# Kernel optimization log

Measured on AMD Instinct MI355X. Metric: run time of the kernel, lower is better.

The kernel has to match this reference:

```python
import jax, jax.numpy as jnp
import numpy as np


def setup_inputs() -> dict:
    key = jax.random.key(0)
    kq, kk, kv = jax.random.split(key, 3)
    B, L, S, H, E, D = 2, 2048, 2048, 16, 64, 64
    return {
        "queries": jax.random.normal(kq, (B, L, H, E), dtype=jnp.float32),
        "keys": jax.random.normal(kk, (B, S, H, E), dtype=jnp.float32),
        "values": jax.random.normal(kv, (B, S, H, D), dtype=jnp.float32),
    }


def reference(queries, keys, values):
    # FullAttention forward (mask_flag=False, dropout=0.0 -> identity)
    E = queries.shape[-1]
    scale = 1.0 / jnp.sqrt(jnp.asarray(E, dtype=queries.dtype))
    # scores: [B, H, L, S]
    scores = jnp.einsum('blhe,bshe->bhls', queries, keys)
    A = jax.nn.softmax(scale * scores, axis=-1)
    # output: [B, L, H, D]
    V = jnp.einsum('bhls,bshd->blhd', A, values)
    return V
```

## Files before the change

### kernel.cpp

```cpp
#include <hip/hip_runtime.h>
#include <hip/hip_bf16.h>
#include <string.h>


#define NB 2
#define LL 2048
#define SS 2048
#define HH 16
#define EE 64
#define DD 64
#define KVB 64
#define NT (SS / KVB)
#define NWG2 (NB * HH * (LL / 64))

typedef _Float16 f16x8 __attribute__((ext_vector_type(8)));
typedef float f32x4 __attribute__((ext_vector_type(4)));
typedef float f32x16 __attribute__((ext_vector_type(16)));
typedef unsigned uint2v __attribute__((ext_vector_type(2)));
typedef unsigned uint4v __attribute__((ext_vector_type(4)));
typedef const __attribute__((address_space(1))) void* gas_p;
typedef __attribute__((address_space(3))) void* las_p;

__device__ __forceinline__ unsigned pk2h(float a, float b) {
    auto h = __builtin_amdgcn_cvt_pkrtz(a, b);
    unsigned u;
    __builtin_memcpy(&u, &h, 4);
    return u;
}

__device__ __forceinline__ float fexp2(float x) {
#if defined(__has_builtin) && __has_builtin(__builtin_amdgcn_exp2f)
    return __builtin_amdgcn_exp2f(x);
#else
    return exp2f(x);
#endif
}

__device__ __forceinline__ void gll16(const void* g, void* l) {
    __builtin_amdgcn_global_load_lds((gas_p)g, (las_p)l, 16, 0, 0);
}

__device__ __forceinline__ uint2v plswap(unsigned a, unsigned b) {
#if defined(__has_builtin) && __has_builtin(__builtin_amdgcn_permlane32_swap)
    return __builtin_amdgcn_permlane32_swap(a, b, false, false);
#else
    unsigned ax = (unsigned)__shfl_xor((int)a, 32);
    unsigned bx = (unsigned)__shfl_xor((int)b, 32);
    int l32 = (int)(threadIdx.x & 32);
    uint2v r;
    r[0] = l32 ? bx : a;
    r[1] = l32 ? b : ax;
    return r;
#endif
}

__device__ __forceinline__ float fbits(unsigned u) {
    float f; __builtin_memcpy(&f, &u, 4); return f;
}
__device__ __forceinline__ unsigned ubits(float f) {
    unsigned u; __builtin_memcpy(&u, &f, 4); return u;
}
__device__ __forceinline__ float xsum32(float x) {
    uint2v r = plswap(ubits(x), ubits(x));
    return fbits(r[0]) + fbits(r[1]);
}

__global__ __launch_bounds__(256) void prepKV(const float* __restrict__ K,
                                              const float* __restrict__ V,
                                              unsigned short* __restrict__ Kh,
                                              unsigned short* __restrict__ Vth) {
    const int NTILE = NB * HH * NT;
    const bool isV = blockIdx.x >= NTILE;
    const int tile = blockIdx.x & (NTILE - 1);
    const int it = tile & (NT - 1);
    const int bh = tile >> 5;
    const int b = bh >> 4, h = bh & 15;
    const int t = threadIdx.x;

    if (!isV) {
        const int s = t >> 2, ec = t & 3;
        const float* src = K + (((size_t)b * SS + it * KVB + s) * HH + h) * EE + ec * 16;
        f32x4 x0 = ((const f32x4*)src)[0];
        f32x4 x1 = ((const f32x4*)src)[1];
        f32x4 x2 = ((const f32x4*)src)[2];
        f32x4 x3 = ((const f32x4*)src)[3];
        uint4v c0, c1;
        c0.x = pk2h(x0[0], x0[1]); c0.y = pk2h(x0[2], x0[3]);
        c0.z = pk2h(x1[0], x1[1]); c0.w = pk2h(x1[2], x1[3]);
        c1.x = pk2h(x2[0], x2[1]); c1.y = pk2h(x2[2], x2[3]);
        c1.z = pk2h(x3[0], x3[1]); c1.w = pk2h(x3[2], x3[3]);
        char* dst = (char*)Kh + (size_t)tile * 8192;
        const int sw = (s & 7) << 4;
        *(uint4v*)(dst + ((s * 128 + ec * 32) ^ sw)) = c0;
        *(uint4v*)(dst + ((s * 128 + ec * 32 + 16) ^ sw)) = c1;
    } else {
        __shared__ float Vt[64 * 68];
        {
            const int s = t >> 2, dc = t & 3;
            const float* src = V + (((size_t)b * SS + it * KVB + s) * HH + h) * DD + dc * 16;
            f32x4 x0 = ((const f32x4*)src)[0];
            f32x4 x1 = ((const f32x4*)src)[1];
            f32x4 x2 = ((const f32x4*)src)[2];
            f32x4 x3 = ((const f32x4*)src)[3];
            float* row = Vt + s * 68 + dc * 16;
            ((f32x4*)row)[0] = x0; ((f32x4*)row)[1] = x1;
            ((f32x4*)row)[2] = x2; ((f32x4*)row)[3] = x3;
        }
        __syncthreads();
        {
            const int d = t >> 2, sc = t & 3;
            float w[16];
#pragma unroll
            for (int j = 0; j < 16; ++j) w[j] = Vt[(sc * 16 + j) * 68 + d];
            uint4v c0, c1;
            c0.x = pk2h(w[0], w[1]); c0.y = pk2h(w[2], w[3]);
            c0.z = pk2h(w[4], w[5]); c0.w = pk2h(w[6], w[7]);
            c1.x = pk2h(w[8], w[9]); c1.y = pk2h(w[10], w[11]);
            c1.z = pk2h(w[12], w[13]); c1.w = pk2h(w[14], w[15]);
            char* dst = (char*)Vth + (size_t)tile * 8192;
            const int sw = (d & 7) << 4;
            *(uint4v*)(dst + ((d * 128 + sc * 32) ^ sw)) = c0;
            *(uint4v*)(dst + ((d * 128 + sc * 32 + 16) ^ sw)) = c1;
        }
    }
}

__global__ __launch_bounds__(256, 4) void fattn9(const unsigned short* __restrict__ Kh,
                                                 const unsigned short* __restrict__ Vth,
                                                 const float* __restrict__ Q,
                                                 float* __restrict__ O) {
    __shared__ __align__(16) char LB[32768];
    __shared__ float lsh[4][32];
    char* K0s = LB;
    char* K1s = LB + 8192;
    char* V0s = LB + 16384;
    char* V1s = LB + 24576;

    const int tid = threadIdx.x;
    const int lane = tid & 63;
    const int wid = tid >> 6;
    const int ln = lane & 31;
    const int hi = lane >> 5;
    const int qg = wid >> 1;
    const int sh = wid & 1;

    const int bid0 = blockIdx.x;
    const int bid = (bid0 & 7) * (NWG2 >> 3) + (bid0 >> 3);
    const int bh = bid >> 5;
    const int qt = bid & 31;
    const int b = bh >> 4, h = bh & 15;
    const int qrow = qt * 64 + qg * 32 + ln;

    const float qs = 0.125f * 1.44269504088896340736f;
    const float* qptr = Q + (((size_t)b * LL + qrow) * HH + h) * EE + hi * 8;
    f16x8 qf[4];
#pragma unroll
    for (int ks = 0; ks < 4; ++ks) {
        f32x4 a0 = *(const f32x4*)(qptr + ks * 16);
        f32x4 a1 = *(const f32x4*)(qptr + ks * 16 + 4);
        union { f16x8 v; unsigned u[4]; } cv;
        cv.u[0] = pk2h(a0[0] * qs, a0[1] * qs);
        cv.u[1] = pk2h(a0[2] * qs, a0[3] * qs);
        cv.u[2] = pk2h(a1[0] * qs, a1[1] * qs);
        cv.u[3] = pk2h(a1[2] * qs, a1[3] * qs);
        qf[ks] = cv.v;
    }

    f32x16 o0, o1;
#pragma unroll
    for (int i = 0; i < 16; ++i) { o0[i] = 0.f; o1[i] = 0.f; }
    float l = 0.f;

    const char* Kg = (const char*)Kh + (size_t)bh * (NT * 8192);
    const char* Vg = (const char*)Vth + (size_t)bh * (NT * 8192);

    auto STAGE = [&](int it, char* Ks, char* Vs) {
        const size_t off = (size_t)it * 8192 + wid * 2048 + lane * 16;
        gll16(Kg + off, Ks + wid * 2048);
        gll16(Kg + off + 1024, Ks + wid * 2048 + 1024);
        gll16(Vg + off, Vs + wid * 2048);
        gll16(Vg + off + 1024, Vs + wid * 2048 + 1024);
    };

    const int swz = (ln & 7) << 4;
    const int srow = sh * 32 + ln;
    const int vcol = sh * 64;

    auto COMPUTE = [&](const char* Ks, const char* Vs) {
        f32x16 st;
#pragma unroll
        for (int i = 0; i < 16; ++i) st[i] = 0.f;
        __builtin_amdgcn_s_setprio(1);
#pragma unroll
        for (int ks = 0; ks < 4; ++ks) {
            f16x8 kf = *(const f16x8*)(Ks + ((srow * 128 + ks * 32 + hi * 16) ^ swz));
            st = __builtin_amdgcn_mfma_f32_32x32x16_f16(kf, qf[ks], st, 0, 0, 0);
        }
        __builtin_amdgcn_s_setprio(0);

        float t0 = 0.f, t1 = 0.f, t2 = 0.f, t3 = 0.f;
#pragma unroll
        for (int r = 0; r < 16; r += 4) {
            st[r] = fexp2(st[r]);
            st[r + 1] = fexp2(st[r + 1]);
            st[r + 2] = fexp2(st[r + 2]);
            st[r + 3] = fexp2(st[r + 3]);
            t0 += st[r]; t1 += st[r + 1]; t2 += st[r + 2]; t3 += st[r + 3];
        }
        l += (t0 + t1) + (t2 + t3);

        {
            uint2v r0 = plswap(pk2h(st[0], st[1]), pk2h(st[4], st[5]));
            uint2v r1 = plswap(pk2h(st[2], st[3]), pk2h(st[6], st[7]));
            union { f16x8 v; unsigned u[4]; } w;
            w.u[0] = r0[0]; w.u[1] = r1[0]; w.u[2] = r0[1]; w.u[3] = r1[1];
            f16x8 v0 = *(const f16x8*)(Vs + ((ln * 128 + vcol + hi * 16) ^ swz));
            f16x8 v1 = *(const f16x8*)(Vs + (((32 + ln) * 128 + vcol + hi * 16) ^ swz));
            __builtin_amdgcn_s_setprio(1);
            o0 = __builtin_amdgcn_mfma_f32_32x32x16_f16(v0, w.v, o0, 0, 0, 0);
            o1 = __builtin_amdgcn_mfma_f32_32x32x16_f16(v1, w.v, o1, 0, 0, 0);
            __builtin_amdgcn_s_setprio(0);
        }
        {
            uint2v r2 = plswap(pk2h(st[8], st[9]), pk2h(st[12], st[13]));
            uint2v r3 = plswap(pk2h(st[10], st[11]), pk2h(st[14], st[15]));
            union { f16x8 v; unsigned u[4]; } w;
            w.u[0] = r2[0]; w.u[1] = r3[0]; w.u[2] = r2[1]; w.u[3] = r3[1];
            f16x8 v0 = *(const f16x8*)(Vs + ((ln * 128 + vcol + 32 + hi * 16) ^ swz));
            f16x8 v1 = *(const f16x8*)(Vs + (((32 + ln) * 128 + vcol + 32 + hi * 16) ^ swz));
            __builtin_amdgcn_s_setprio(1);
            o0 = __builtin_amdgcn_mfma_f32_32x32x16_f16(v0, w.v, o0, 0, 0, 0);
            o1 = __builtin_amdgcn_mfma_f32_32x32x16_f16(v1, w.v, o1, 0, 0, 0);
            __builtin_amdgcn_s_setprio(0);
        }
    };

    STAGE(0, K0s, V0s);
    __syncthreads();
    for (int it = 0; it < NT; it += 2) {
        if (it + 1 < NT) STAGE(it + 1, K1s, V1s);
        COMPUTE(K0s, V0s);
        __syncthreads();
        if (it + 2 < NT) STAGE(it + 2, K0s, V0s);
        COMPUTE(K1s, V1s);
        __syncthreads();
    }

    l = xsum32(l);
    if (hi == 0) lsh[wid][ln] = l;
    __syncthreads();
    const float lo = lsh[wid ^ 1][ln];
    const float lstar = l + lo;

    float* pbuf = (float*)LB + qg * (32 * 65);
    if (sh == 1) {
#pragma unroll
        for (int r = 0; r < 16; ++r) {
            const int d = (r & 3) + 8 * (r >> 2) + 4 * hi;
            pbuf[ln * 65 + d] = o0[r];
            pbuf[ln * 65 + 32 + d] = o1[r];
        }
    }
    __syncthreads();
    if (sh == 0) {
        const float invl = 1.f / lstar;
        float* optr = O + (((size_t)b * LL + qrow) * HH + h) * DD;
#pragma unroll
        for (int t = 0; t < 4; ++t) {
            f32x4 w0, w1;
#pragma unroll
            for (int i = 0; i < 4; ++i) {
                const int d = t * 8 + hi * 4 + i;
                w0[i] = (o0[4 * t + i] + pbuf[ln * 65 + d]) * invl;
                w1[i] = (o1[4 * t + i] + pbuf[ln * 65 + 32 + d]) * invl;
            }
            *(f32x4*)(optr + t * 8 + hi * 4) = w0;
            *(f32x4*)(optr + 32 + t * 8 + hi * 4) = w1;
        }
    }
}

typedef unsigned u2f __attribute__((ext_vector_type(2)));
__global__ __launch_bounds__(256) void fattn1(const float* __restrict__ Q,
                                              const float* __restrict__ K,
                                              const float* __restrict__ V,
                                              float* __restrict__ O) {
    __shared__ __align__(16) short Klds[KVB * 64];
    __shared__ __align__(16) short Vtlds[64 * KVB];
    __shared__ __align__(16) short Plds[4][16 * 64];

    const int tid = threadIdx.x;
    const int lane = tid & 63;
    const int wid = tid >> 6;
    const int g = (lane >> 4) & 3;
    const int c = lane & 15;

    const int bid = blockIdx.x;
    const int bh = bid >> 5;
    const int qt = bid & 31;
    const int b = bh >> 4;
    const int h = bh & 15;
    const int q0 = qt * 64;

    const int qrow = q0 + wid * 16 + c;
    const float* qptr = Q + (((size_t)b * LL + qrow) * HH + h) * EE;
    const float qs = 0.125f * 1.44269504088896340736f;
    f16x8 qf[2];
#pragma unroll
    for (int kk = 0; kk < 2; ++kk) {
        f32x4 a0 = *(const f32x4*)(qptr + kk * 32 + g * 8);
        f32x4 a1 = *(const f32x4*)(qptr + kk * 32 + g * 8 + 4);
        union { f16x8 v; unsigned u[4]; } cv;
        cv.u[0] = pk2h(a0[0] * qs, a0[1] * qs);
        cv.u[1] = pk2h(a0[2] * qs, a0[3] * qs);
        cv.u[2] = pk2h(a1[0] * qs, a1[1] * qs);
        cv.u[3] = pk2h(a1[2] * qs, a1[3] * qs);
        qf[kk] = cv.v;
    }

    f32x4 osacc[4];
    const f32x4 fzero = {0.f, 0.f, 0.f, 0.f};
#pragma unroll
    for (int i = 0; i < 4; ++i) osacc[i] = fzero;
    float m_run = -1e30f;
    float l_run = 0.f;

    const int km = tid & 15;
    const int kr = tid >> 4;

    for (int it = 0; it < NT; ++it) {
        const int s_glob = it * KVB;
        f32x4 kreg[4];
#pragma unroll
        for (int p = 0; p < 4; ++p) {
            int s = kr + p * 16;
            kreg[p] = *(const f32x4*)(K + (((size_t)b * SS + s_glob + s) * HH + h) * EE + km * 4);
        }
        f32x4 vreg[4];
#pragma unroll
        for (int p = 0; p < 4; ++p) {
            int s = kr * 4 + p;
            vreg[p] = *(const f32x4*)(V + (((size_t)b * SS + s_glob + s) * HH + h) * DD + km * 4);
        }
        __syncthreads();
#pragma unroll
        for (int p = 0; p < 4; ++p) {
            int s = kr + p * 16;
            u2f w;
            w.x = pk2h(kreg[p][0], kreg[p][1]);
            w.y = pk2h(kreg[p][2], kreg[p][3]);
            int byte = (s * 128 + km * 8) ^ ((s & 7) << 4);
            *(u2f*)((char*)Klds + byte) = w;
        }
#pragma unroll
        for (int i = 0; i < 4; ++i) {
            int d = km * 4 + i;
            u2f w;
            w.x = pk2h(vreg[0][i], vreg[1][i]);
            w.y = pk2h(vreg[2][i], vreg[3][i]);
            int byte = (d * 128 + kr * 8) ^ ((d & 7) << 4);
            *(u2f*)((char*)Vtlds + byte) = w;
        }
        __syncthreads();

        f32x4 stv[4];
#pragma unroll
        for (int fr = 0; fr < 4; ++fr) stv[fr] = fzero;
#pragma unroll
        for (int fr = 0; fr < 4; ++fr) {
            int s = fr * 16 + c;
            f16x8 kf0 = *(const f16x8*)((const char*)Klds + ((s * 128 + 16 * g) ^ ((s & 7) << 4)));
            stv[fr] = __builtin_amdgcn_mfma_f32_16x16x32_f16(kf0, qf[0], stv[fr], 0, 0, 0);
            f16x8 kf1 = *(const f16x8*)((const char*)Klds + ((s * 128 + 64 + 16 * g) ^ ((s & 7) << 4)));
            stv[fr] = __builtin_amdgcn_mfma_f32_16x16x32_f16(kf1, qf[1], stv[fr], 0, 0, 0);
        }

        float pmax = stv[0][0];
#pragma unroll
        for (int fr = 0; fr < 4; ++fr)
#pragma unroll
            for (int r = 0; r < 4; ++r) pmax = fmaxf(pmax, stv[fr][r]);
        pmax = fmaxf(pmax, __shfl_xor(pmax, 16));
        pmax = fmaxf(pmax, __shfl_xor(pmax, 32));
        float mnew = fmaxf(m_run, pmax);
        float alpha = fexp2(m_run - mnew);
        float tsum = 0.f;
#pragma unroll
        for (int fr = 0; fr < 4; ++fr)
#pragma unroll
            for (int r = 0; r < 4; ++r) {
                float e = fexp2(stv[fr][r] - mnew);
                stv[fr][r] = e;
                tsum += e;
            }
        tsum += __shfl_xor(tsum, 16);
        tsum += __shfl_xor(tsum, 32);
        l_run = l_run * alpha + tsum;
        m_run = mnew;
#pragma unroll
        for (int fr = 0; fr < 4; ++fr)
#pragma unroll
            for (int r = 0; r < 4; ++r) osacc[fr][r] *= alpha;

        short* plb = &Plds[wid][0];
#pragma unroll
        for (int fr = 0; fr < 4; ++fr) {
            u2f w;
            w.x = pk2h(stv[fr][0], stv[fr][1]);
            w.y = pk2h(stv[fr][2], stv[fr][3]);
            int byte = (c * 128 + fr * 32 + g * 8) ^ ((c & 7) << 4);
            *(u2f*)((char*)plb + byte) = w;
        }
        f16x8 pb0 = *(const f16x8*)((const char*)plb + ((c * 128 + 16 * g) ^ ((c & 7) << 4)));
        f16x8 pb1 = *(const f16x8*)((const char*)plb + ((c * 128 + 64 + 16 * g) ^ ((c & 7) << 4)));

#pragma unroll
        for (int fr = 0; fr < 4; ++fr) {
            int d = fr * 16 + c;
            f16x8 vf0 = *(const f16x8*)((const char*)Vtlds + ((d * 128 + 16 * g) ^ ((d & 7) << 4)));
            osacc[fr] = __builtin_amdgcn_mfma_f32_16x16x32_f16(vf0, pb0, osacc[fr], 0, 0, 0);
            f16x8 vf1 = *(const f16x8*)((const char*)Vtlds + ((d * 128 + 64 + 16 * g) ^ ((d & 7) << 4)));
            osacc[fr] = __builtin_amdgcn_mfma_f32_16x16x32_f16(vf1, pb1, osacc[fr], 0, 0, 0);
        }
    }

    float invl = 1.f / l_run;
    float* optr = O + (((size_t)b * LL + qrow) * HH + h) * DD;
#pragma unroll
    for (int fr = 0; fr < 4; ++fr) {
        f32x4 o;
        o[0] = osacc[fr][0] * invl;
        o[1] = osacc[fr][1] * invl;
        o[2] = osacc[fr][2] * invl;
        o[3] = osacc[fr][3] * invl;
        *(f32x4*)(optr + fr * 16 + g * 4) = o;
    }
}

extern "C" void kernel_launch(void* const* d_in, const int* in_sizes, int n_in,
                              void* d_out, int out_size, void* d_ws, size_t ws_size,
                              hipStream_t stream) {
    const float* Q = (const float*)d_in[0];
    const float* K = (const float*)d_in[1];
    const float* V = (const float*)d_in[2];
    float* Op = (float*)d_out;

    const size_t halfBytes = (size_t)NB * HH * SS * EE * 2;
    if (ws_size >= 2 * halfBytes) {
        unsigned short* Kht = (unsigned short*)d_ws;
        unsigned short* Vht = (unsigned short*)((char*)d_ws + halfBytes);
        hipLaunchKernelGGL(prepKV, dim3(2 * NB * HH * NT), dim3(256), 0, stream, K, V, Kht, Vht);
        hipLaunchKernelGGL(fattn9, dim3(NWG2), dim3(256), 0, stream, Kht, Vht, Q, Op);
    } else {
        hipLaunchKernelGGL(fattn1, dim3(NB * HH * (LL / 64)), dim3(256), 0, stream, Q, K, V, Op);
    }
}
```

Measured before the change: 61.86 us.

## Read V tiles directly from global memory instead of staging through LDS

Stops staging V tiles into shared memory. Each wave now loads its swizzled V fragments straight from global memory inside the compute step, and the LDS buffer shrinks to hold only the double-buffered K tiles. The V loads and all four K fragment loads are issued up front, before the QK MFMA chain, so their latency can overlap the math. The aim is to cut LDS traffic and footprint for better occupancy, at the cost of higher-latency global loads on the critical path and possibly redundant V reads across waves.

```diff
diff --git a/kernel.cpp b/kernel.cpp
--- a/kernel.cpp
+++ b/kernel.cpp
@@ -125,16 +125,14 @@
     }
 }
 
-__global__ __launch_bounds__(256, 4) void fattn9(const unsigned short* __restrict__ Kh,
-                                                 const unsigned short* __restrict__ Vth,
-                                                 const float* __restrict__ Q,
-                                                 float* __restrict__ O) {
-    __shared__ __align__(16) char LB[32768];
+__global__ __launch_bounds__(256, 4) void fattn11(const unsigned short* __restrict__ Kh,
+                                                  const unsigned short* __restrict__ Vth,
+                                                  const float* __restrict__ Q,
+                                                  float* __restrict__ O) {
+    __shared__ __align__(16) char LB[16640];
     __shared__ float lsh[4][32];
-    char* K0s = LB;
-    char* K1s = LB + 8192;
-    char* V0s = LB + 16384;
-    char* V1s = LB + 24576;
+    char* KA = LB;
+    char* KB = LB + 8192;
 
     const int tid = threadIdx.x;
     const int lane = tid & 63;
@@ -167,35 +165,43 @@
     }
 
     f32x16 o0, o1;
-#pragma unroll
-    for (int i = 0; i < 16; ++i) { o0[i] = 0.f; o1[i] = 0.f; }
+    f32x16 zs;
+#pragma unroll
+    for (int i = 0; i < 16; ++i) { o0[i] = 0.f; o1[i] = 0.f; zs[i] = 0.f; }
     float l = 0.f;
 
     const char* Kg = (const char*)Kh + (size_t)bh * (NT * 8192);
     const char* Vg = (const char*)Vth + (size_t)bh * (NT * 8192);
 
-    auto STAGE = [&](int it, char* Ks, char* Vs) {
+    auto STAGE_K = [&](int it, char* Ks) {
         const size_t off = (size_t)it * 8192 + wid * 2048 + lane * 16;
         gll16(Kg + off, Ks + wid * 2048);
         gll16(Kg + off + 1024, Ks + wid * 2048 + 1024);
-        gll16(Vg + off, Vs + wid * 2048);
-        gll16(Vg + off + 1024, Vs + wid * 2048 + 1024);
     };
 
     const int swz = (ln & 7) << 4;
     const int srow = sh * 32 + ln;
     const int vcol = sh * 64;
-
-    auto COMPUTE = [&](const char* Ks, const char* Vs) {
-        f32x16 st;
-#pragma unroll
-        for (int i = 0; i < 16; ++i) st[i] = 0.f;
+    const int vo00 = (ln * 128 + vcol + hi * 16) ^ swz;
+    const int vo01 = ((32 + ln) * 128 + vcol + hi * 16) ^ swz;
+    const int vo10 = (ln * 128 + vcol + 32 + hi * 16) ^ swz;
+    const int vo11 = ((32 + ln) * 128 + vcol + 32 + hi * 16) ^ swz;
+
+    auto COMPUTE = [&](const char* Ks, const char* vtile) {
+        f16x8 v00 = *(const f16x8*)(vtile + vo00);
+        f16x8 v01 = *(const f16x8*)(vtile + vo01);
+        f16x8 v10 = *(const f16x8*)(vtile + vo10);
+        f16x8 v11 = *(const f16x8*)(vtile + vo11);
+
+        f16x8 k0 = *(const f16x8*)(Ks + ((srow * 128 + 0 * 32 + hi * 16) ^ swz));
+        f16x8 k1 = *(const f16x8*)(Ks + ((srow * 128 + 1 * 32 + hi * 16) ^ swz));
+        f16x8 k2 = *(const f16x8*)(Ks + ((srow * 128 + 2 * 32 + hi * 16) ^ swz));
+        f16x8 k3 = *(const f16x8*)(Ks + ((srow * 128 + 3 * 32 + hi * 16) ^ swz));
         __builtin_amdgcn_s_setprio(1);
-#pragma unroll
-        for (int ks = 0; ks < 4; ++ks) {
-            f16x8 kf = *(const f16x8*)(Ks + ((srow * 128 + ks * 32 + hi * 16) ^ swz));
-            st = __builtin_amdgcn_mfma_f32_32x32x16_f16(kf, qf[ks], st, 0, 0, 0);
-        }
+        f32x16 st = __builtin_amdgcn_mfma_f32_32x32x16_f16(k0, qf[0], zs, 0, 0, 0);
+        st = __builtin_amdgcn_mfma_f32_32x32x16_f16(k1, qf[1], st, 0, 0, 0);
+        st = __builtin_amdgcn_mfma_f32_32x32x16_f16(k2, qf[2], st, 0, 0, 0);
+        st = __builtin_amdgcn_mfma_f32_32x32x16_f16(k3, qf[3], st, 0, 0, 0);
         __builtin_amdgcn_s_setprio(0);
 
         float t0 = 0.f, t1 = 0.f, t2 = 0.f, t3 = 0.f;
@@ -214,11 +220,9 @@
             uint2v r1 = plswap(pk2h(st[2], st[3]), pk2h(st[6], st[7]));
             union { f16x8 v; unsigned u[4]; } w;
             w.u[0] = r0[0]; w.u[1] = r1[0]; w.u[2] = r0[1]; w.u[3] = r1[1];
-            f16x8 v0 = *(const f16x8*)(Vs + ((ln * 128 + vcol + hi * 16) ^ swz));
-            f16x8 v1 = *(const f16x8*)(Vs + (((32 + ln) * 128 + vcol + hi * 16) ^ swz));
             __builtin_amdgcn_s_setprio(1);
-            o0 = __builtin_amdgcn_mfma_f32_32x32x16_f16(v0, w.v, o0, 0, 0, 0);
-            o1 = __builtin_amdgcn_mfma_f32_32x32x16_f16(v1, w.v, o1, 0, 0, 0);
+            o0 = __builtin_amdgcn_mfma_f32_32x32x16_f16(v00, w.v, o0, 0, 0, 0);
+            o1 = __builtin_amdgcn_mfma_f32_32x32x16_f16(v01, w.v, o1, 0, 0, 0);
             __builtin_amdgcn_s_setprio(0);
         }
         {
@@ -226,23 +230,21 @@
             uint2v r3 = plswap(pk2h(st[10], st[11]), pk2h(st[14], st[15]));
             union { f16x8 v; unsigned u[4]; } w;
             w.u[0] = r2[0]; w.u[1] = r3[0]; w.u[2] = r2[1]; w.u[3] = r3[1];
-            f16x8 v0 = *(const f16x8*)(Vs + ((ln * 128 + vcol + 32 + hi * 16) ^ swz));
-            f16x8 v1 = *(const f16x8*)(Vs + (((32 + ln) * 128 + vcol + 32 + hi * 16) ^ swz));
             __builtin_amdgcn_s_setprio(1);
-            o0 = __builtin_amdgcn_mfma_f32_32x32x16_f16(v0, w.v, o0, 0, 0, 0);
-            o1 = __builtin_amdgcn_mfma_f32_32x32x16_f16(v1, w.v, o1, 0, 0, 0);
+            o0 = __builtin_amdgcn_mfma_f32_32x32x16_f16(v10, w.v, o0, 0, 0, 0);
+            o1 = __builtin_amdgcn_mfma_f32_32x32x16_f16(v11, w.v, o1, 0, 0, 0);
             __builtin_amdgcn_s_setprio(0);
         }
     };
 
-    STAGE(0, K0s, V0s);
+    STAGE_K(0, KA);
     __syncthreads();
-    for (int it = 0; it < NT; it += 2) {
-        if (it + 1 < NT) STAGE(it + 1, K1s, V1s);
-        COMPUTE(K0s, V0s);
+    for (int t = 0; t < NT; t += 2) {
+        if (t + 1 < NT) STAGE_K(t + 1, KB);
+        COMPUTE(KA, Vg + (size_t)t * 8192);
         __syncthreads();
-        if (it + 2 < NT) STAGE(it + 2, K0s, V0s);
-        COMPUTE(K1s, V1s);
+        if (t + 2 < NT) STAGE_K(t + 2, KA);
+        COMPUTE(KB, Vg + (size_t)(t + 1) * 8192);
         __syncthreads();
     }
 
@@ -450,7 +452,7 @@
         unsigned short* Kht = (unsigned short*)d_ws;
         unsigned short* Vht = (unsigned short*)((char*)d_ws + halfBytes);
         hipLaunchKernelGGL(prepKV, dim3(2 * NB * HH * NT), dim3(256), 0, stream, K, V, Kht, Vht);
-        hipLaunchKernelGGL(fattn9, dim3(NWG2), dim3(256), 0, stream, Kht, Vht, Q, Op);
+        hipLaunchKernelGGL(fattn11, dim3(NWG2), dim3(256), 0, stream, Kht, Vht, Q, Op);
     } else {
         hipLaunchKernelGGL(fattn1, dim3(NB * HH * (LL / 64)), dim3(256), 0, stream, Q, K, V, Op);
     }
```

Result: slower. 65.42 us (+5.8%).
